# Kernel optimization log

Hardware: AMD Instinct MI355X
Metric: run time of the kernel (lower is better)

The kernel has to match this reference:

```python
import jax, jax.numpy as jnp
import numpy as np

HIDDEN = 512
STATE_DIM = 256
H = 8
D = STATE_DIM // H  # 32
B = 8
T = 4096


def setup_inputs() -> dict:
    key = jax.random.key(0)
    ks = jax.random.split(key, 12)
    s = 0.02
    return {
        "hidden_states": jax.random.normal(ks[0], (B, T, HIDDEN), jnp.float32),
        "state": jnp.zeros((B, H, D, D), jnp.float32),
        "W_k": jax.random.normal(ks[1], (STATE_DIM, HIDDEN), jnp.float32) * s,
        "W_v": jax.random.normal(ks[2], (STATE_DIM, HIDDEN), jnp.float32) * s,
        "W_q": jax.random.normal(ks[3], (STATE_DIM, HIDDEN), jnp.float32) * s,
        "W_beta": jax.random.normal(ks[4], (STATE_DIM, HIDDEN), jnp.float32) * s,
        "b_beta": jnp.zeros((STATE_DIM,), jnp.float32),
        "W_alpha": jax.random.normal(ks[5], (STATE_DIM, HIDDEN), jnp.float32) * s,
        "b_alpha": jnp.full((STATE_DIM,), 2.0, jnp.float32),
        "W_out": jax.random.normal(ks[6], (HIDDEN, STATE_DIM), jnp.float32) * s,
        "gate_W": jax.random.normal(ks[7], (STATE_DIM, HIDDEN), jnp.float32) * s,
        "norm_w": jnp.ones((STATE_DIM,), jnp.float32),
    }


def _rms_norm(x, w, eps=1e-6):
    dtype = x.dtype
    xf = x.astype(jnp.float32)
    n = xf * jax.lax.rsqrt(jnp.mean(xf * xf, axis=-1, keepdims=True) + eps)
    return (n * w).astype(dtype)


def reference(hidden_states, state, W_k, W_v, W_q, W_beta, b_beta, W_alpha, b_alpha, W_out, gate_W, norm_w):
    bsz, seq_len, _ = hidden_states.shape
    # projections -> (B, T, H, D)
    k = (hidden_states @ W_k.T).reshape(bsz, seq_len, H, D)
    v = (hidden_states @ W_v.T).reshape(bsz, seq_len, H, D)
    q = (hidden_states @ W_q.T).reshape(bsz, seq_len, H, D)
    beta = jax.nn.sigmoid(hidden_states @ W_beta.T + b_beta).reshape(bsz, seq_len, H, D)
    alpha = jax.nn.sigmoid(hidden_states @ W_alpha.T + b_alpha).reshape(bsz, seq_len, H, D)
    # F.normalize(k, dim=-1) with eps=1e-12
    k = k / jnp.maximum(jnp.linalg.norm(k, axis=-1, keepdims=True), 1e-12)
    gate = hidden_states @ gate_W.T  # (B, T, STATE_DIM)

    # time-major for scan: (T, B, H, D)
    def tm(x):
        return jnp.swapaxes(x, 0, 1)

    def step(S, inp):
        k_t, v_t, q_t, b_t, a_t = inp
        S = S * a_t[..., None]                              # row-wise decay
        pred = jnp.einsum('bhij,bhj->bhi', S, k_t)
        S = S + jnp.einsum('bhi,bhj->bhij', b_t * (v_t - pred), k_t)
        readout = jnp.einsum('bhij,bhj->bhi', S, q_t)       # (B, H, D)
        return S, readout

    S_final, readouts = jax.lax.scan(step, state, (tm(k), tm(v), tm(q), tm(beta), tm(alpha)))
    context = jnp.swapaxes(readouts, 0, 1).reshape(bsz, seq_len, STATE_DIM)
    context = _rms_norm(context, norm_w) * jax.nn.silu(gate)
    output = context @ W_out.T
    return output, S_final
```

## Files before the change

kernel.cpp:

```cpp
#include <hip/hip_runtime.h>
#include <stdint.h>

#define B_    8
#define T_    4096
#define HID   512
#define SD    256
#define NH    8
#define HD    32
#define M_TOK (B_*T_)

typedef __attribute__((ext_vector_type(8))) short short8;
typedef __attribute__((ext_vector_type(4))) float f32x4;
typedef __attribute__((ext_vector_type(4))) float f4;
typedef __attribute__((ext_vector_type(2))) float f2;

__device__ __forceinline__ unsigned short f2bf(float f) {
  uint32_t u = __float_as_uint(f);
  uint32_t r = (u + 0x7fffu + ((u >> 16) & 1u)) >> 16;
  return (unsigned short)r;
}

__device__ __forceinline__ void gload16(const void* g, void* l) {
  __builtin_amdgcn_global_load_lds((const __attribute__((address_space(1))) void*)g,
                                   (__attribute__((address_space(3))) void*)l,
                                   16, 0, 0);
}

__device__ __forceinline__ float qred16(float x) {
  x += __int_as_float(__builtin_amdgcn_mov_dpp(__float_as_int(x), 0xB1,  0xF, 0xF, true));
  x += __int_as_float(__builtin_amdgcn_mov_dpp(__float_as_int(x), 0x4E,  0xF, 0xF, true));
  x += __int_as_float(__builtin_amdgcn_mov_dpp(__float_as_int(x), 0x141, 0xF, 0xF, true));
  x += __int_as_float(__builtin_amdgcn_mov_dpp(__float_as_int(x), 0x128, 0xF, 0xF, true));
  return x;
}

__device__ __forceinline__ float dpp_xor1(float x) {
  return __int_as_float(__builtin_amdgcn_mov_dpp(__float_as_int(x), 0xB1, 0xF, 0xF, true));
}

__global__ void cvt_f32_bf16(const float* __restrict__ in, unsigned short* __restrict__ out, int n4) {
  int i = blockIdx.x * blockDim.x + threadIdx.x;
  int stride = gridDim.x * blockDim.x;
  for (; i < n4; i += stride) {
    float4 v = reinterpret_cast<const float4*>(in)[i];
    ushort4 o;
    o.x = f2bf(v.x); o.y = f2bf(v.y); o.z = f2bf(v.z); o.w = f2bf(v.w);
    reinterpret_cast<ushort4*>(out)[i] = o;
  }
}

__global__ void __launch_bounds__(256) cvt_weights(
    const float* __restrict__ W_k, const float* __restrict__ W_v,
    const float* __restrict__ W_q, const float* __restrict__ W_beta,
    const float* __restrict__ W_alpha, const float* __restrict__ gate_W,
    const float* __restrict__ W_out,
    unsigned short* __restrict__ Wc, unsigned short* __restrict__ Wob)
{
  int slice = blockIdx.y;
  const float* src = (slice == 0) ? W_k : (slice == 1) ? W_v : (slice == 2) ? W_q :
                     (slice == 3) ? W_beta : (slice == 4) ? W_alpha : (slice == 5) ? gate_W : W_out;
  unsigned short* dst = (slice == 6) ? Wob : (Wc + slice * 131072);
  int i = blockIdx.x * 256 + threadIdx.x;
  float4 v = reinterpret_cast<const float4*>(src)[i];
  ushort4 o;
  o.x = f2bf(v.x); o.y = f2bf(v.y); o.z = f2bf(v.z); o.w = f2bf(v.w);
  reinterpret_cast<ushort4*>(dst)[i] = o;
}

#define PM 128
#define PN 64
#define PK 64

__global__ void __launch_bounds__(256) proj_gemm(
    const unsigned short* __restrict__ hb, const unsigned short* __restrict__ Wc,
    const float* __restrict__ b_beta, const float* __restrict__ b_alpha,
    float* __restrict__ KQi, float* __restrict__ AVBf, float* __restrict__ gate)
{
  __shared__ unsigned short Asm[PM*PK];
  __shared__ unsigned short Bsm[3][PN*PK];
  const int t = threadIdx.x;
  const int w = t >> 6, lane = t & 63;
  const int bm0 = blockIdx.x * PM;
  const int role = blockIdx.y;
  const int grp = role >> 2;
  const int bn0 = (role & 3) * 64;
  const int pr0 = grp ? 4 : 0, pr1 = grp ? 1 : 2, pr2 = grp ? 3 : 5;

  f32x4 acc[3][2][4];
  #pragma unroll
  for (int pp = 0; pp < 3; ++pp)
    #pragma unroll
    for (int i = 0; i < 2; ++i)
      #pragma unroll
      for (int j = 0; j < 4; ++j) acc[pp][i][j] = (f32x4){0.f, 0.f, 0.f, 0.f};

  for (int k0 = 0; k0 < HID; k0 += PK) {
    #pragma unroll
    for (int it = 0; it < 4; ++it) {
      int unit = t + it * 256;
      int row = unit >> 3, seg = unit & 7;
      int dseg = seg ^ (row & 7);
      const unsigned short* g = hb + (size_t)(bm0 + row) * HID + k0 + dseg * 8;
      gload16(g, (char*)Asm + (w * 1024 + it * 4096));
    }
    #pragma unroll
    for (int pp = 0; pp < 3; ++pp) {
      const int pr = (pp == 0) ? pr0 : (pp == 1) ? pr1 : pr2;
      #pragma unroll
      for (int it = 0; it < 2; ++it) {
        int unit = t + it * 256;
        int n = unit >> 3, seg = unit & 7;
        int dseg = seg ^ (n & 7);
        const unsigned short* g = Wc + (size_t)(pr * 256 + bn0 + n) * HID + k0 + dseg * 8;
        gload16(g, (char*)Bsm[pp] + (w * 1024 + it * 4096));
      }
    }
    __syncthreads();
    #pragma unroll
    for (int ks = 0; ks < 2; ++ks) {
      short8 af[2];
      int u = ks * 4 + (lane >> 4);
      int slot = u ^ (lane & 7);
      #pragma unroll
      for (int rb = 0; rb < 2; ++rb) {
        int row = w * 32 + rb * 16 + (lane & 15);
        af[rb] = *(const short8*)((const char*)Asm + row * 128 + slot * 16);
      }
      #pragma unroll
      for (int pp = 0; pp < 3; ++pp) {
        short8 bfr[4];
        #pragma unroll
        for (int cb = 0; cb < 4; ++cb) {
          int nn = cb * 16 + (lane & 15);
          bfr[cb] = *(const short8*)((const char*)Bsm[pp] + nn * 128 + slot * 16);
        }
        #pragma unroll
        for (int rb = 0; rb < 2; ++rb)
          #pragma unroll
          for (int cb = 0; cb < 4; ++cb)
            acc[pp][rb][cb] = __builtin_amdgcn_mfma_f32_16x16x32_bf16(af[rb], bfr[cb], acc[pp][rb][cb], 0, 0, 0);
      }
    }
    __syncthreads();
  }

  if (grp == 0) {
    #pragma unroll
    for (int rb = 0; rb < 2; ++rb) {
      #pragma unroll
      for (int r = 0; r < 4; ++r) {
        float s0 = acc[0][rb][0][r] * acc[0][rb][0][r] + acc[0][rb][1][r] * acc[0][rb][1][r];
        float s1 = acc[0][rb][2][r] * acc[0][rb][2][r] + acc[0][rb][3][r] * acc[0][rb][3][r];
        s0 = qred16(s0); s1 = qred16(s1);
        float i0 = 1.0f / fmaxf(sqrtf(s0), 1e-12f);
        float i1 = 1.0f / fmaxf(sqrtf(s1), 1e-12f);
        acc[0][rb][0][r] *= i0; acc[0][rb][1][r] *= i0;
        acc[0][rb][2][r] *= i1; acc[0][rb][3][r] *= i1;
      }
    }
    #pragma unroll
    for (int rb = 0; rb < 2; ++rb) {
      #pragma unroll
      for (int cb = 0; cb < 4; ++cb) {
        int rem = bn0 + cb * 16 + (lane & 15);
        int h = rem >> 5, d = rem & 31;
        #pragma unroll
        for (int r = 0; r < 4; ++r) {
          int m = bm0 + w * 32 + rb * 16 + (lane >> 4) * 4 + r;
          int bb = m >> 12, tt = m & 4095;
          size_t tok = ((size_t)(bb * NH + h) * T_ + tt);
          float kv = acc[0][rb][cb][r], qv = acc[1][rb][cb][r];
          float kn = dpp_xor1(kv), qn = dpp_xor1(qv);
          if ((lane & 1) == 0)
            *(float4*)&KQi[tok * 64 + (d >> 1) * 4] = (float4){kv, kn, qv, qn};
          gate[(size_t)m * SD + rem] = acc[2][rb][cb][r];
        }
      }
    }
  } else {
    #pragma unroll
    for (int rb = 0; rb < 2; ++rb) {
      #pragma unroll
      for (int cb = 0; cb < 4; ++cb) {
        int rem = bn0 + cb * 16 + (lane & 15);
        int h = rem >> 5, d = rem & 31;
        #pragma unroll
        for (int r = 0; r < 4; ++r) {
          int m = bm0 + w * 32 + rb * 16 + (lane >> 4) * 4 + r;
          int bb = m >> 12, tt = m & 4095;
          size_t tok = ((size_t)(bb * NH + h) * T_ + tt);
          float av = 1.0f / (1.0f + expf(-(acc[0][rb][cb][r] + b_alpha[rem])));
          float vv = acc[1][rb][cb][r];
          float bv = 1.0f / (1.0f + expf(-(acc[2][rb][cb][r] + b_beta[rem])));
          *(float4*)&AVBf[(tok * HD + d) * 4] = (float4){av, vv, bv, 0.0f};
        }
      }
    }
  }
}

#define CH 32
#define NCH (T_/CH)

#define DSR(dst, areg, imm) \
  asm volatile("ds_read_b128 %0, %1 offset:%c2" : "=v"(dst) : "v"(areg), "i"(imm))

#define SHUF2(V,A,B) __builtin_shufflevector(V, V, A, B)

#define BAR asm volatile("s_barrier" ::: "memory")

__global__ void __launch_bounds__(128, 1) scan_kernel(
    const float* __restrict__ KQi, const float4* __restrict__ AVB,
    const float* __restrict__ state_in,
    float* __restrict__ ctx, float* __restrict__ Sfin)
{
  __shared__ __align__(16) char Lds[20480];
  const int blk = blockIdx.x;
  const int bh = blk & 63, rg = blk >> 6;
  const int b = bh >> 3, h = bh & 7;
  const int tid = threadIdx.x;
  const int wid = tid >> 6;
  const int lw = tid & 63;

  const float*  KQg = KQi + (size_t)bh * (T_ * 64);
  const float4* Vg  = AVB + (size_t)bh * (T_ * HD) + rg * 4;

  const uint32_t lds0 = (uint32_t)(uintptr_t)(__attribute__((address_space(3))) char*)&Lds[0];

  if (wid == 1) {
    const int gpp = lw >> 2, gqt = lw & 3;
    f4 gx0, gx1, gx2, gx3, gy0, gy1, gy2, gy3;
    const uint32_t a_gw = lds0 + 16384 + (2 * gpp) * 64 + gqt * 16 + 12;

    auto stageW = [&](int c2, int buf) {
      const float* kqg = KQg + (size_t)c2 * (CH * 64);
      #pragma unroll
      for (int it = 0; it < 8; ++it)
        gload16(kqg + (size_t)(lw + it * 64) * 4, Lds + buf * 8192 + it * 1024);
      const float4* vg = Vg + (size_t)c2 * (CH * HD);
      #pragma unroll
      for (int it = 0; it < 2; ++it) {
        int tc = it * 16 + (lw >> 2), r = lw & 3;
        gload16(vg + (size_t)tc * HD + r, Lds + 16384 + buf * 2048 + it * 1024);
      }
    };

    auto gfetch = [&](int c2) {
      const float* gp = KQg + ((size_t)c2 * CH + 2 * gpp) * 64 + gqt * 16;
      gx0 = *(const f4*)(gp);      gx1 = *(const f4*)(gp + 4);
      gx2 = *(const f4*)(gp + 8);  gx3 = *(const f4*)(gp + 12);
      gy0 = *(const f4*)(gp + 64); gy1 = *(const f4*)(gp + 68);
      gy2 = *(const f4*)(gp + 72); gy3 = *(const f4*)(gp + 76);
    };

    auto gwrite = [&](int buf) {
      f2 g2 = SHUF2(gx0, 0, 1) * SHUF2(gy0, 0, 1);
      g2 = __builtin_elementwise_fma(SHUF2(gx1, 0, 1), SHUF2(gy1, 0, 1), g2);
      g2 = __builtin_elementwise_fma(SHUF2(gx2, 0, 1), SHUF2(gy2, 0, 1), g2);
      g2 = __builtin_elementwise_fma(SHUF2(gx3, 0, 1), SHUF2(gy3, 0, 1), g2);
      float G = g2.x + g2.y;
      G += __int_as_float(__builtin_amdgcn_mov_dpp(__float_as_int(G), 0xB1, 0xF, 0xF, true));
      G += __int_as_float(__builtin_amdgcn_mov_dpp(__float_as_int(G), 0x4E, 0xF, 0xF, true));
      uint32_t aw = a_gw + buf * 2048;
      asm volatile("ds_write_b32 %0, %1" :: "v"(aw), "v"(G));
      asm volatile("s_waitcnt lgkmcnt(0)" ::: "memory");
    };

    gfetch(0);
    stageW(0, 0);
    asm volatile("s_waitcnt vmcnt(0)" ::: "memory");
    gwrite(0);
    BAR;
    #pragma unroll 1
    for (int c = 0; c < NCH; ++c) {
      if (c + 1 < NCH) {
        gfetch(c + 1);
        stageW(c + 1, (c + 1) & 1);
        asm volatile("s_waitcnt vmcnt(0)" ::: "memory");
        gwrite((c + 1) & 1);
      }
      BAR;
    }
    return;
  }

  const int il = lw >> 4;
  const int p  = lw & 15;

  f2 S2;
  {
    const float* sp = state_in + (size_t)bh * 1024 + (rg * 4 + il) * 32 + p * 2;
    S2 = (f2){sp[0], sp[1]};
  }

  const uint32_t a_kq = lds0 + p * 16;
  const uint32_t a_v  = lds0 + 16384 + il * 16;

  float osel = 0.0f;
  float* ctxp = ctx + (size_t)b * T_ * SD + (size_t)p * SD + h * HD + rg * 4 + il;

  f4 kqA, vvA, kqB, vvB, kqC, vvC, kqD, vvD;

#define R2(X, Y, BUF, J) do { \
    DSR(kq##X, a_kq, (BUF)*8192 + (2*(J))*256); \
    DSR(vv##X, a_v,  (BUF)*2048 + (2*(J))*64); \
    DSR(kq##Y, a_kq, (BUF)*8192 + (2*(J)+1)*256); \
    DSR(vv##Y, a_v,  (BUF)*2048 + (2*(J)+1)*64); \
  } while (0)

#define WKA2(N, X, Y) \
    asm volatile("s_waitcnt lgkmcnt(" #N ")" \
                 : "+v"(kq##X), "+v"(vv##X), "+v"(kq##Y), "+v"(vv##Y))

#define C2(X, Y, T0) do { \
    f2 k0_ = SHUF2(kq##X, 0, 1), q0_ = SHUF2(kq##X, 2, 3); \
    f2 k1_ = SHUF2(kq##Y, 0, 1), q1_ = SHUF2(kq##Y, 2, 3); \
    f4 VA_ = vv##X, VB_ = vv##Y; \
    f2 dA_ = k0_ * S2, dB_ = k1_ * S2; \
    float W0_ = qred16(dA_.x + dA_.y); \
    float W1_ = qred16(dB_.x + dB_.y); \
    float u0_ = fmaf(-(VA_.z * VA_.x), W0_, VA_.z * VA_.y); \
    float bua_ = VB_.z * VB_.x; \
    float c2_ = bua_ * VA_.w; \
    float c1_ = fmaf(-(bua_ * VA_.x), W1_, VB_.z * VB_.y); \
    float u1_ = fmaf(-c2_, u0_, c1_); \
    f2 St_ = __builtin_elementwise_fma((f2){u0_, u0_}, k0_, (f2){VA_.x, VA_.x} * S2); \
    f2 Su_ = __builtin_elementwise_fma((f2){u1_, u1_}, k1_, (f2){VB_.x, VB_.x} * St_); \
    f2 o0_ = q0_ * St_; \
    f2 o1_ = q1_ * Su_; \
    S2 = Su_; \
    float od0_ = qred16(o0_.x + o0_.y); \
    float od1_ = qred16(o1_.x + o1_.y); \
    osel = (p == ((T0) & 15))       ? od0_ : osel; \
    osel = (p == (((T0) + 1) & 15)) ? od1_ : osel; \
    if ((((T0) + 1) & 15) == 15) { *ctxp = osel; ctxp += 16 * SD; } \
  } while (0)

#define CHUNK(BUF) do { \
    R2(A,B,BUF,0); R2(C,D,BUF,1); \
    WKA2(4,A,B); C2(A,B, 0); R2(A,B,BUF,2); \
    WKA2(4,C,D); C2(C,D, 2); R2(C,D,BUF,3); \
    WKA2(4,A,B); C2(A,B, 4); R2(A,B,BUF,4); \
    WKA2(4,C,D); C2(C,D, 6); R2(C,D,BUF,5); \
    WKA2(4,A,B); C2(A,B, 8); R2(A,B,BUF,6); \
    WKA2(4,C,D); C2(C,D,10); R2(C,D,BUF,7); \
    WKA2(4,A,B); C2(A,B,12); R2(A,B,BUF,8); \
    WKA2(4,C,D); C2(C,D,14); R2(C,D,BUF,9); \
    WKA2(4,A,B); C2(A,B,16); R2(A,B,BUF,10); \
    WKA2(4,C,D); C2(C,D,18); R2(C,D,BUF,11); \
    WKA2(4,A,B); C2(A,B,20); R2(A,B,BUF,12); \
    WKA2(4,C,D); C2(C,D,22); R2(C,D,BUF,13); \
    WKA2(4,A,B); C2(A,B,24); R2(A,B,BUF,14); \
    WKA2(4,C,D); C2(C,D,26); R2(C,D,BUF,15); \
    WKA2(4,A,B); C2(A,B,28); \
    WKA2(0,C,D); C2(C,D,30); \
    BAR; \
  } while (0)

  BAR;
  #pragma unroll 1
  for (int cp = 0; cp < NCH / 2; ++cp) {
    CHUNK(0);
    CHUNK(1);
  }

  {
    float* sp = Sfin + (size_t)bh * 1024 + (rg * 4 + il) * 32 + p * 2;
    sp[0] = S2.x; sp[1] = S2.y;
  }
#undef C2
#undef R2
#undef WKA2
#undef CHUNK
}

__global__ void __launch_bounds__(256) rms_silu(
    const float* __restrict__ ctx, const float* __restrict__ gate,
    const float* __restrict__ norm_w, unsigned short* __restrict__ ctx2)
{
  size_t row = (size_t)blockIdx.x * 4 + (threadIdx.x >> 6);
  int lane = threadIdx.x & 63;
  const float4 x = *(const float4*)&ctx[row * SD + lane * 4];
  float s = x.x * x.x + x.y * x.y + x.z * x.z + x.w * x.w;
  #pragma unroll
  for (int m = 32; m >= 1; m >>= 1) s += __shfl_xor(s, m, 64);
  float rs = 1.0f / sqrtf(s * (1.0f / 256.0f) + 1e-6f);
  const float4 g = *(const float4*)&gate[row * SD + lane * 4];
  const float4 w = *(const float4*)&norm_w[lane * 4];
  ushort4 o;
  o.x = f2bf(x.x * rs * w.x * (g.x / (1.0f + expf(-g.x))));
  o.y = f2bf(x.y * rs * w.y * (g.y / (1.0f + expf(-g.y))));
  o.z = f2bf(x.z * rs * w.z * (g.z / (1.0f + expf(-g.z))));
  o.w = f2bf(x.w * rs * w.w * (g.w / (1.0f + expf(-g.w))));
  *(ushort4*)&ctx2[row * SD + lane * 4] = o;
}

__global__ void __launch_bounds__(256) out_gemm(
    const unsigned short* __restrict__ ctx2, const unsigned short* __restrict__ Wob,
    float* __restrict__ out)
{
  __shared__ unsigned short Asm[PM*PK];
  __shared__ unsigned short Bsm[PN*PK];
  const int t = threadIdx.x;
  const int w = t >> 6, lane = t & 63;
  const int bm0 = blockIdx.x * PM;
  const int bn0 = blockIdx.y * PN;

  f32x4 acc[2][4];
  #pragma unroll
  for (int i = 0; i < 2; ++i)
    #pragma unroll
    for (int j = 0; j < 4; ++j) acc[i][j] = (f32x4){0.f, 0.f, 0.f, 0.f};

  for (int k0 = 0; k0 < SD; k0 += PK) {
    #pragma unroll
    for (int it = 0; it < 4; ++it) {
      int unit = t + it * 256;
      int row = unit >> 3, seg = unit & 7;
      int dseg = seg ^ (row & 7);
      const unsigned short* g = ctx2 + (size_t)(bm0 + row) * SD + k0 + dseg * 8;
      gload16(g, (char*)Asm + (w * 1024 + it * 4096));
    }
    #pragma unroll
    for (int it = 0; it < 2; ++it) {
      int unit = t + it * 256;
      int n = unit >> 3, seg = unit & 7;
      int dseg = seg ^ (n & 7);
      const unsigned short* g = Wob + (size_t)(bn0 + n) * SD + k0 + dseg * 8;
      gload16(g, (char*)Bsm + (w * 1024 + it * 4096));
    }
    __syncthreads();
    #pragma unroll
    for (int ks = 0; ks < 2; ++ks) {
      short8 af[2], bfr[4];
      int u = ks * 4 + (lane >> 4);
      int slot = u ^ (lane & 7);
      #pragma unroll
      for (int rb = 0; rb < 2; ++rb) {
        int row = w * 32 + rb * 16 + (lane & 15);
        af[rb] = *(const short8*)((const char*)Asm + row * 128 + slot * 16);
      }
      #pragma unroll
      for (int cb = 0; cb < 4; ++cb) {
        int nn = cb * 16 + (lane & 15);
        bfr[cb] = *(const short8*)((const char*)Bsm + nn * 128 + slot * 16);
      }
      #pragma unroll
      for (int rb = 0; rb < 2; ++rb)
        #pragma unroll
        for (int cb = 0; cb < 4; ++cb)
          acc[rb][cb] = __builtin_amdgcn_mfma_f32_16x16x32_bf16(af[rb], bfr[cb], acc[rb][cb], 0, 0, 0);
    }
    __syncthreads();
  }
  #pragma unroll
  for (int rb = 0; rb < 2; ++rb)
    #pragma unroll
    for (int cb = 0; cb < 4; ++cb) {
      int n = bn0 + cb * 16 + (lane & 15);
      #pragma unroll
      for (int r = 0; r < 4; ++r) {
        int m = bm0 + w * 32 + rb * 16 + (lane >> 4) * 4 + r;
        out[(size_t)m * 512 + n] = acc[rb][cb][r];
      }
    }
}

extern "C" void kernel_launch(void* const* d_in, const int* in_sizes, int n_in,
                              void* d_out, int out_size, void* d_ws, size_t ws_size,
                              hipStream_t stream) {
  (void)in_sizes; (void)n_in; (void)out_size; (void)ws_size;
  const float* hidden  = (const float*)d_in[0];
  const float* state   = (const float*)d_in[1];
  const float* W_k     = (const float*)d_in[2];
  const float* W_v     = (const float*)d_in[3];
  const float* W_q     = (const float*)d_in[4];
  const float* W_beta  = (const float*)d_in[5];
  const float* b_beta  = (const float*)d_in[6];
  const float* W_alpha = (const float*)d_in[7];
  const float* b_alpha = (const float*)d_in[8];
  const float* W_out   = (const float*)d_in[9];
  const float* gate_W  = (const float*)d_in[10];
  const float* norm_w  = (const float*)d_in[11];
  float* out = (float*)d_out;

  char* ws = (char*)d_ws;
  unsigned short* hb  = (unsigned short*)(ws);
  unsigned short* Wc  = (unsigned short*)(ws + 33554432);
  unsigned short* Wob = (unsigned short*)(ws + 35127296);
  float* KQi  = (float*)(ws + 35389440);
  float* AVBf = (float*)(ws + 102498304);
  unsigned short* ctx2 = (unsigned short*)(ws + 236716032);
  float* ctx  = out;
  float* gate = out + 8388608;
  float* Sfin = out + 16777216;

  cvt_f32_bf16<<<2048, 256, 0, stream>>>(hidden, hb, M_TOK * HID / 4);
  cvt_weights<<<dim3(128, 7), 256, 0, stream>>>(W_k, W_v, W_q, W_beta, W_alpha, gate_W, W_out, Wc, Wob);

  proj_gemm<<<dim3(256, 8), 256, 0, stream>>>(hb, Wc, b_beta, b_alpha, KQi, AVBf, gate);
  scan_kernel<<<512, 128, 0, stream>>>(KQi, (const float4*)AVBf, state, ctx, Sfin);
  rms_silu<<<8192, 256, 0, stream>>>(ctx, gate, norm_w, ctx2);
  out_gemm<<<dim3(256, 8), 256, 0, stream>>>(ctx2, Wob, out);
}
```

Baseline: 401.5 us.

## Drop LDS staging wave in scan; load operands directly from global with prefetch

```diff
diff --git a/kernel.cpp b/kernel.cpp
--- a/kernel.cpp
+++ b/kernel.cpp
@@ -199,93 +199,30 @@
   }
 }
 
-#define CH 32
-#define NCH (T_/CH)
-
-#define DSR(dst, areg, imm) \
-  asm volatile("ds_read_b128 %0, %1 offset:%c2" : "=v"(dst) : "v"(areg), "i"(imm))
+#define NPAIR (T_/2)
+
+#define GLDO(dst, ptr, imm) \
+  asm volatile("global_load_dwordx4 %0, %1, off offset:%c2" : "=v"(dst) : "v"(ptr), "i"(imm))
+
+#define STG(ptr, val) \
+  asm volatile("global_store_dword %0, %1, off" :: "v"(ptr), "v"(val) : "memory")
 
 #define SHUF2(V,A,B) __builtin_shufflevector(V, V, A, B)
 
-#define BAR asm volatile("s_barrier" ::: "memory")
-
-__global__ void __launch_bounds__(128, 1) scan_kernel(
-    const float* __restrict__ KQi, const float4* __restrict__ AVB,
+__global__ void __launch_bounds__(64, 1) scan_kernel(
+    const float* __restrict__ KQi, const float* __restrict__ AVBf,
     const float* __restrict__ state_in,
     float* __restrict__ ctx, float* __restrict__ Sfin)
 {
-  __shared__ __align__(16) char Lds[20480];
   const int blk = blockIdx.x;
   const int bh = blk & 63, rg = blk >> 6;
   const int b = bh >> 3, h = bh & 7;
-  const int tid = threadIdx.x;
-  const int wid = tid >> 6;
-  const int lw = tid & 63;
-
-  const float*  KQg = KQi + (size_t)bh * (T_ * 64);
-  const float4* Vg  = AVB + (size_t)bh * (T_ * HD) + rg * 4;
-
-  const uint32_t lds0 = (uint32_t)(uintptr_t)(__attribute__((address_space(3))) char*)&Lds[0];
-
-  if (wid == 1) {
-    const int gpp = lw >> 2, gqt = lw & 3;
-    f4 gx0, gx1, gx2, gx3, gy0, gy1, gy2, gy3;
-    const uint32_t a_gw = lds0 + 16384 + (2 * gpp) * 64 + gqt * 16 + 12;
-
-    auto stageW = [&](int c2, int buf) {
-      const float* kqg = KQg + (size_t)c2 * (CH * 64);
-      #pragma unroll
-      for (int it = 0; it < 8; ++it)
-        gload16(kqg + (size_t)(lw + it * 64) * 4, Lds + buf * 8192 + it * 1024);
-      const float4* vg = Vg + (size_t)c2 * (CH * HD);
-      #pragma unroll
-      for (int it = 0; it < 2; ++it) {
-        int tc = it * 16 + (lw >> 2), r = lw & 3;
-        gload16(vg + (size_t)tc * HD + r, Lds + 16384 + buf * 2048 + it * 1024);
-      }
-    };
-
-    auto gfetch = [&](int c2) {
-      const float* gp = KQg + ((size_t)c2 * CH + 2 * gpp) * 64 + gqt * 16;
-      gx0 = *(const f4*)(gp);      gx1 = *(const f4*)(gp + 4);
-      gx2 = *(const f4*)(gp + 8);  gx3 = *(const f4*)(gp + 12);
-      gy0 = *(const f4*)(gp + 64); gy1 = *(const f4*)(gp + 68);
-      gy2 = *(const f4*)(gp + 72); gy3 = *(const f4*)(gp + 76);
-    };
-
-    auto gwrite = [&](int buf) {
-      f2 g2 = SHUF2(gx0, 0, 1) * SHUF2(gy0, 0, 1);
-      g2 = __builtin_elementwise_fma(SHUF2(gx1, 0, 1), SHUF2(gy1, 0, 1), g2);
-      g2 = __builtin_elementwise_fma(SHUF2(gx2, 0, 1), SHUF2(gy2, 0, 1), g2);
-      g2 = __builtin_elementwise_fma(SHUF2(gx3, 0, 1), SHUF2(gy3, 0, 1), g2);
-      float G = g2.x + g2.y;
-      G += __int_as_float(__builtin_amdgcn_mov_dpp(__float_as_int(G), 0xB1, 0xF, 0xF, true));
-      G += __int_as_float(__builtin_amdgcn_mov_dpp(__float_as_int(G), 0x4E, 0xF, 0xF, true));
-      uint32_t aw = a_gw + buf * 2048;
-      asm volatile("ds_write_b32 %0, %1" :: "v"(aw), "v"(G));
-      asm volatile("s_waitcnt lgkmcnt(0)" ::: "memory");
-    };
-
-    gfetch(0);
-    stageW(0, 0);
-    asm volatile("s_waitcnt vmcnt(0)" ::: "memory");
-    gwrite(0);
-    BAR;
-    #pragma unroll 1
-    for (int c = 0; c < NCH; ++c) {
-      if (c + 1 < NCH) {
-        gfetch(c + 1);
-        stageW(c + 1, (c + 1) & 1);
-        asm volatile("s_waitcnt vmcnt(0)" ::: "memory");
-        gwrite((c + 1) & 1);
-      }
-      BAR;
-    }
-    return;
-  }
-
+  const int lw = threadIdx.x;
   const int il = lw >> 4;
   const int p  = lw & 15;
+
+  const float* kp = KQi  + (size_t)bh * (T_ * 64) + p * 4;
+  const float* vp = AVBf + (size_t)bh * (T_ * 128) + (rg * 4 + il) * 4;
 
   f2 S2;
   {
@@ -293,35 +230,35 @@
     S2 = (f2){sp[0], sp[1]};
   }
 
-  const uint32_t a_kq = lds0 + p * 16;
-  const uint32_t a_v  = lds0 + 16384 + il * 16;
-
   float osel = 0.0f;
   float* ctxp = ctx + (size_t)b * T_ * SD + (size_t)p * SD + h * HD + rg * 4 + il;
 
   f4 kqA, vvA, kqB, vvB, kqC, vvC, kqD, vvD;
-
-#define R2(X, Y, BUF, J) do { \
-    DSR(kq##X, a_kq, (BUF)*8192 + (2*(J))*256); \
-    DSR(vv##X, a_v,  (BUF)*2048 + (2*(J))*64); \
-    DSR(kq##Y, a_kq, (BUF)*8192 + (2*(J)+1)*256); \
-    DSR(vv##Y, a_v,  (BUF)*2048 + (2*(J)+1)*64); \
+  f4 kqE, vvE, kqF, vvF, kqG, vvG, kqH, vvH;
+
+#define R2G(X, Y) do { \
+    GLDO(kq##X, kp, 0); \
+    GLDO(vv##X, vp, 0); \
+    GLDO(kq##Y, kp, 256); \
+    GLDO(vv##Y, vp, 512); \
+    kp += 128; vp += 256; \
   } while (0)
 
-#define WKA2(N, X, Y) \
-    asm volatile("s_waitcnt lgkmcnt(" #N ")" \
+#define WV(N, X, Y) \
+    asm volatile("s_waitcnt vmcnt(" #N ")" \
                  : "+v"(kq##X), "+v"(vv##X), "+v"(kq##Y), "+v"(vv##Y))
 
 #define C2(X, Y, T0) do { \
     f2 k0_ = SHUF2(kq##X, 0, 1), q0_ = SHUF2(kq##X, 2, 3); \
     f2 k1_ = SHUF2(kq##Y, 0, 1), q1_ = SHUF2(kq##Y, 2, 3); \
     f4 VA_ = vv##X, VB_ = vv##Y; \
-    f2 dA_ = k0_ * S2, dB_ = k1_ * S2; \
+    f2 dA_ = k0_ * S2, dB_ = k1_ * S2, dG_ = k0_ * k1_; \
     float W0_ = qred16(dA_.x + dA_.y); \
     float W1_ = qred16(dB_.x + dB_.y); \
+    float G_  = qred16(dG_.x + dG_.y); \
     float u0_ = fmaf(-(VA_.z * VA_.x), W0_, VA_.z * VA_.y); \
     float bua_ = VB_.z * VB_.x; \
-    float c2_ = bua_ * VA_.w; \
+    float c2_ = bua_ * G_; \
     float c1_ = fmaf(-(bua_ * VA_.x), W1_, VB_.z * VB_.y); \
     float u1_ = fmaf(-c2_, u0_, c1_); \
     f2 St_ = __builtin_elementwise_fma((f2){u0_, u0_}, k0_, (f2){VA_.x, VA_.x} * S2); \
@@ -333,45 +270,38 @@
     float od1_ = qred16(o1_.x + o1_.y); \
     osel = (p == ((T0) & 15))       ? od0_ : osel; \
     osel = (p == (((T0) + 1) & 15)) ? od1_ : osel; \
-    if ((((T0) + 1) & 15) == 15) { *ctxp = osel; ctxp += 16 * SD; } \
+    if ((((T0) + 1) & 15) == 15) { STG(ctxp, osel); ctxp += 16 * SD; } \
   } while (0)
 
-#define CHUNK(BUF) do { \
-    R2(A,B,BUF,0); R2(C,D,BUF,1); \
-    WKA2(4,A,B); C2(A,B, 0); R2(A,B,BUF,2); \
-    WKA2(4,C,D); C2(C,D, 2); R2(C,D,BUF,3); \
-    WKA2(4,A,B); C2(A,B, 4); R2(A,B,BUF,4); \
-    WKA2(4,C,D); C2(C,D, 6); R2(C,D,BUF,5); \
-    WKA2(4,A,B); C2(A,B, 8); R2(A,B,BUF,6); \
-    WKA2(4,C,D); C2(C,D,10); R2(C,D,BUF,7); \
-    WKA2(4,A,B); C2(A,B,12); R2(A,B,BUF,8); \
-    WKA2(4,C,D); C2(C,D,14); R2(C,D,BUF,9); \
-    WKA2(4,A,B); C2(A,B,16); R2(A,B,BUF,10); \
-    WKA2(4,C,D); C2(C,D,18); R2(C,D,BUF,11); \
-    WKA2(4,A,B); C2(A,B,20); R2(A,B,BUF,12); \
-    WKA2(4,C,D); C2(C,D,22); R2(C,D,BUF,13); \
-    WKA2(4,A,B); C2(A,B,24); R2(A,B,BUF,14); \
-    WKA2(4,C,D); C2(C,D,26); R2(C,D,BUF,15); \
-    WKA2(4,A,B); C2(A,B,28); \
-    WKA2(0,C,D); C2(C,D,30); \
-    BAR; \
-  } while (0)
-
-  BAR;
+  R2G(A,B); R2G(C,D); R2G(E,F); R2G(G,H);
+
   #pragma unroll 1
-  for (int cp = 0; cp < NCH / 2; ++cp) {
-    CHUNK(0);
-    CHUNK(1);
-  }
+  for (int it = 0; it < (NPAIR - 8) / 8; ++it) {
+    WV(12,A,B); C2(A,B, 0); R2G(A,B);
+    WV(12,C,D); C2(C,D, 2); R2G(C,D);
+    WV(12,E,F); C2(E,F, 4); R2G(E,F);
+    WV(12,G,H); C2(G,H, 6); R2G(G,H);
+    WV(12,A,B); C2(A,B, 8); R2G(A,B);
+    WV(12,C,D); C2(C,D,10); R2G(C,D);
+    WV(12,E,F); C2(E,F,12); R2G(E,F);
+    WV(12,G,H); C2(G,H,14); R2G(G,H);
+  }
+  WV(12,A,B); C2(A,B, 0); R2G(A,B);
+  WV(12,C,D); C2(C,D, 2); R2G(C,D);
+  WV(12,E,F); C2(E,F, 4); R2G(E,F);
+  WV(12,G,H); C2(G,H, 6); R2G(G,H);
+  WV(12,A,B); C2(A,B, 8);
+  WV(8 ,C,D); C2(C,D,10);
+  WV(4 ,E,F); C2(E,F,12);
+  WV(0 ,G,H); C2(G,H,14);
 
   {
     float* sp = Sfin + (size_t)bh * 1024 + (rg * 4 + il) * 32 + p * 2;
     sp[0] = S2.x; sp[1] = S2.y;
   }
 #undef C2
-#undef R2
-#undef WKA2
-#undef CHUNK
+#undef R2G
+#undef WV
 }
 
 __global__ void __launch_bounds__(256) rms_silu(
@@ -499,7 +429,7 @@
   cvt_weights<<<dim3(128, 7), 256, 0, stream>>>(W_k, W_v, W_q, W_beta, W_alpha, gate_W, W_out, Wc, Wob);
 
   proj_gemm<<<dim3(256, 8), 256, 0, stream>>>(hb, Wc, b_beta, b_alpha, KQi, AVBf, gate);
-  scan_kernel<<<512, 128, 0, stream>>>(KQi, (const float4*)AVBf, state, ctx, Sfin);
+  scan_kernel<<<512, 64, 0, stream>>>(KQi, AVBf, state, ctx, Sfin);
   rms_silu<<<8192, 256, 0, stream>>>(ctx, gate, norm_w, ctx2);
   out_gemm<<<dim3(256, 8), 256, 0, stream>>>(ctx2, Wob, out);
 }
```

After: 578.4 us. 1.44x slower.
